# Performance work log

Measured on AMD Instinct MI355X. Metric: run time of the kernel, lower is better.

The kernel has to match this reference:

```python
import jax, jax.numpy as jnp
import numpy as np

HEADS = 8
DIM_HEAD = 64
SCALE = DIM_HEAD ** -0.5


def setup_inputs() -> dict:
    key = jax.random.key(0)
    k1, k2, k3, k4 = jax.random.split(key, 4)
    b, dim, l = 4, 512, 2048
    hidden = HEADS * DIM_HEAD  # 512
    x = jax.random.normal(k1, (b, dim, l), dtype=jnp.float32)
    w_qkv = jax.random.normal(k2, (3 * hidden, dim), dtype=jnp.float32) * (dim ** -0.5)
    w_out = jax.random.normal(k3, (dim, hidden), dtype=jnp.float32) * (hidden ** -0.5)
    b_out = jax.random.normal(k4, (dim,), dtype=jnp.float32) * 0.01
    return {"x": x, "w_qkv": w_qkv, "w_out": w_out, "b_out": b_out}


def reference(x, w_qkv, w_out, b_out):
    b, c, l = x.shape
    h, d = HEADS, DIM_HEAD
    # 1x1 Conv1d == channel matmul: [3*hidden, c] x [b, c, l] -> [b, 3*hidden, l]
    qkv = jnp.einsum('oc,bcl->bol', w_qkv, x)
    q, k, v = jnp.split(qkv, 3, axis=1)
    # 'b (h d) l -> b h d l'
    q = q.reshape(b, h, d, l) * SCALE
    k = k.reshape(b, h, d, l)
    v = v.reshape(b, h, d, l)
    sim = jnp.einsum('bhdi,bhdj->bhij', q, k)          # [b, h, l, l]
    attn = jax.nn.softmax(sim, axis=-1)
    out = jnp.einsum('bhij,bhdj->bhid', attn, v)       # [b, h, l, d]
    # 'b h l d -> b (h d) l'
    out = out.transpose(0, 1, 3, 2).reshape(b, h * d, l)
    return jnp.einsum('oc,bcl->bol', w_out, out) + b_out[None, :, None]
```

## Files before the change

kernel.cpp:

```cpp
#include <hip/hip_runtime.h>

#define L_SEQ 2048
#define KDIM  512

typedef __attribute__((ext_vector_type(8))) short short8v;
typedef __attribute__((ext_vector_type(4))) float f32x4;

static __device__ __forceinline__ short f2b(float f) {
    union { float f; unsigned u; } v; v.f = f;
    unsigned r = v.u + 0x7fffu + ((v.u >> 16) & 1u);
    return (short)(r >> 16);
}

static __device__ __forceinline__ float fast_exp2(float x) {
#if __has_builtin(__builtin_amdgcn_exp2f)
    return __builtin_amdgcn_exp2f(x);
#else
    return exp2f(x);
#endif
}

static __device__ __forceinline__ void gl2lds16(const short* g, short* l) {
    __builtin_amdgcn_global_load_lds(
        (const __attribute__((address_space(1))) unsigned*)g,
        (__attribute__((address_space(3))) unsigned*)l,
        16, 0, 0);
}

__global__ __launch_bounds__(256) void prep(
    const float* __restrict__ wq, const float* __restrict__ wo,
    const float* __restrict__ x,
    short* __restrict__ wqb, short* __restrict__ wob, short* __restrict__ xT)
{
    __shared__ __align__(16) float T[64 * 72];
    const int t = threadIdx.x;
    int bid = blockIdx.x;

    if (bid < 1024) {
        const int i = bid * 256 + t;
        const int NQ = 1536 * 512 / 4;
        float4 v;
        if (i < NQ) v = ((const float4*)wq)[i];
        else        v = ((const float4*)wo)[i - NQ];
        short4 s;
        s.x = f2b(v.x); s.y = f2b(v.y); s.z = f2b(v.z); s.w = f2b(v.w);
        if (i < NQ) ((short4*)wqb)[i] = s;
        else        ((short4*)wob)[i - NQ] = s;
        return;
    }
    bid -= 1024;
    const int l0 = (bid & 31) * 64;
    const int c0 = ((bid >> 5) & 7) * 64;
    const int b  = bid >> 8;

#pragma unroll
    for (int j = 0; j < 4; ++j) {
        const int idx = j * 256 + t;
        const int row = idx >> 4, c4 = idx & 15;
        const float4 v = *(const float4*)&x[((size_t)b * KDIM + c0 + row) * L_SEQ + l0 + c4 * 4];
        *(float4*)&T[row * 72 + c4 * 4] = v;
    }
    __syncthreads();

#pragma unroll
    for (int j = 0; j < 2; ++j) {
        const int idx = j * 256 + t;
        const int l = idx >> 3, ch = idx & 7;
        short8v s;
#pragma unroll
        for (int e = 0; e < 8; ++e)
            s[e] = f2b(T[(ch * 8 + e) * 72 + l]);
        *(short8v*)&xT[((size_t)b * L_SEQ + l0 + l) * KDIM + c0 + ch * 8] = s;
    }
}

template<int EPI>
__global__ __launch_bounds__(256) void gemm_bt(
    const short* __restrict__ Ag, const short* __restrict__ Bbase,
    const float* __restrict__ bias,
    short* __restrict__ Qws, short* __restrict__ Kws, short* __restrict__ Vws,
    float* __restrict__ Cout)
{
    constexpr int TO   = (EPI == 0) ? 128 : 64;
    constexpr int WO   = TO / 2;
    constexpr int NI   = WO / 16;
    constexpr int CA   = TO * 64 * 2 / 1024;
    constexpr int CB   = 16;
    constexpr int CPW  = (CA + CB) / 4;
    constexpr int SMEM = (EPI == 0) ? 34816 : 24576;

    const int bz = blockIdx.z;
    const int o0 = blockIdx.y * TO;
    const int l0 = blockIdx.x * 128;
    const short* Bg = Bbase + (size_t)bz * L_SEQ * KDIM;

    __shared__ __align__(16) char smem[SMEM];
    short* sA = (short*)smem;
    short* sB = (short*)(smem + TO * 64 * 2);

    const int t    = threadIdx.x;
    const int w    = t >> 6;
    const int lane = t & 63;
    const int quad = lane >> 4;
    const int l16  = lane & 15;
    const int wo   = (w & 1) * WO;
    const int wl   = (w >> 1) * 64;

    f32x4 acc[NI][4];
#pragma unroll
    for (int i = 0; i < NI; ++i)
#pragma unroll
        for (int n = 0; n < 4; ++n) acc[i][n] = (f32x4){0,0,0,0};

    const int lrow = lane >> 3;
    const int lcol = (lane & 7) * 8;

    for (int k0 = 0; k0 < KDIM; k0 += 64) {
#pragma unroll
        for (int p = 0; p < CPW; ++p) {
            const int cid = w * CPW + p;
            if (cid < CA) {
                const int row = cid * 8 + lrow;
                gl2lds16(Ag + (size_t)(o0 + row) * KDIM + k0 + lcol, sA + cid * 512);
            } else {
                const int row = (cid - CA) * 8 + lrow;
                gl2lds16(Bg + (size_t)(l0 + row) * KDIM + k0 + lcol, sB + (cid - CA) * 512);
            }
        }
        __syncthreads();

#pragma unroll
        for (int ks = 0; ks < 2; ++ks) {
            short8v af[NI], bf[4];
#pragma unroll
            for (int i = 0; i < NI; ++i)
                af[i] = *(const short8v*)&sA[(wo + i * 16 + l16) * 64 + ks * 32 + quad * 8];
#pragma unroll
            for (int n = 0; n < 4; ++n)
                bf[n] = *(const short8v*)&sB[(wl + n * 16 + l16) * 64 + ks * 32 + quad * 8];
#pragma unroll
            for (int i = 0; i < NI; ++i)
#pragma unroll
                for (int n = 0; n < 4; ++n)
                    acc[i][n] = __builtin_amdgcn_mfma_f32_16x16x32_bf16(af[i], bf[n], acc[i][n], 0, 0, 0);
        }
        __syncthreads();
    }

    if (EPI == 0) {
        const int type  = o0 >> 9;
        const int local = o0 & 511;
        const int bh0   = bz * 8 + (local >> 6);
        const float sc  = (type == 0) ? 0.18033688011112042f : 1.0f;
        short* T = (short*)smem;

        if (type == 2) {
#pragma unroll
            for (int i = 0; i < NI; ++i)
#pragma unroll
                for (int n = 0; n < 4; ++n)
#pragma unroll
                    for (int r = 0; r < 4; ++r)
                        T[(wo + i * 16 + quad * 4 + r) * 136 + wl + n * 16 + l16] =
                            f2b(acc[i][n][r]);
            __syncthreads();
#pragma unroll
            for (int p = 0; p < 8; ++p) {
                const int idx = p * 256 + t;
                const int o = idx >> 4, c = idx & 15;
                const float4 v = *(const float4*)&T[o * 136 + c * 8];
                short* dst = Vws + ((size_t)(bh0 + (o >> 6)) * 64 + (o & 63)) * L_SEQ + l0 + c * 8;
                *(float4*)dst = v;
            }
        } else {
#pragma unroll
            for (int i = 0; i < NI; ++i)
#pragma unroll
                for (int n = 0; n < 4; ++n) {
                    short4 s;
                    s.x = f2b(acc[i][n][0] * sc);
                    s.y = f2b(acc[i][n][1] * sc);
                    s.z = f2b(acc[i][n][2] * sc);
                    s.w = f2b(acc[i][n][3] * sc);
                    *(short4*)&T[(wl + n * 16 + l16) * 136 + wo + i * 16 + quad * 4] = s;
                }
            __syncthreads();
            short* base = (type == 0) ? Qws : Kws;
#pragma unroll
            for (int p = 0; p < 8; ++p) {
                const int idx = p * 256 + t;
                const int l = idx >> 4, c = idx & 15;
                const float4 v = *(const float4*)&T[l * 136 + c * 8];
                short* dst = base + ((size_t)(bh0 + (c >> 3)) * L_SEQ + l0 + l) * 64 + (c & 7) * 8;
                *(float4*)dst = v;
            }
        }
    } else {
        float* Cb = Cout + (size_t)bz * KDIM * L_SEQ;
#pragma unroll
        for (int i = 0; i < NI; ++i) {
            const int o = o0 + wo + i * 16 + quad * 4;
            float bv[4];
#pragma unroll
            for (int r = 0; r < 4; ++r) bv[r] = bias[o + r];
#pragma unroll
            for (int n = 0; n < 4; ++n) {
                const int l = l0 + wl + n * 16 + l16;
#pragma unroll
                for (int r = 0; r < 4; ++r)
                    Cb[(size_t)(o + r) * L_SEQ + l] = acc[i][n][r] + bv[r];
            }
        }
    }
}

__global__ __launch_bounds__(256) void attn_mfma(
    const short* __restrict__ Qws, const short* __restrict__ Kws,
    const short* __restrict__ Vws, short* __restrict__ ao)
{
    const int bh = blockIdx.x & 31;
    const int b  = bh >> 3;
    const int h  = bh & 7;
    const int i0 = (blockIdx.x >> 5) * 128;

    __shared__ __align__(16) char smem[36864];
    short* Kld = (short*)smem;
    short* Vld = (short*)(smem + 9216);
    short* Pld = (short*)(smem + 18432);
    float* Old = (float*)smem;

    const int t    = threadIdx.x;
    const int w    = t >> 6;
    const int lane = t & 63;
    const int quad = lane >> 4;
    const int l16  = lane & 15;

    const short* Qb = Qws + (size_t)bh * L_SEQ * 64;
    const short* Kb = Kws + (size_t)bh * L_SEQ * 64;
    const short* Vb = Vws + (size_t)bh * 64 * L_SEQ;

    short8v qa[2][2];
#pragma unroll
    for (int hh = 0; hh < 2; ++hh) {
        const short* qrow = Qb + (size_t)(i0 + w * 32 + hh * 16 + l16) * 64 + quad * 8;
        qa[hh][0] = *(const short8v*)qrow;
        qa[hh][1] = *(const short8v*)(qrow + 32);
    }

    f32x4 oacc[2][4];
#pragma unroll
    for (int hh = 0; hh < 2; ++hh)
#pragma unroll
        for (int n = 0; n < 4; ++n) oacc[hh][n] = (f32x4){0,0,0,0};
    float rsum[2] = {0.f, 0.f};
    short* Pw = Pld + w * 32 * 72;

    const int r = t >> 2, c = t & 3;

    for (int j0 = 0; j0 < L_SEQ; j0 += 64) {
        {
            const float4 k0 = *(const float4*)(Kb + (size_t)(j0 + r) * 64 + c * 16);
            const float4 k1 = *(const float4*)(Kb + (size_t)(j0 + r) * 64 + c * 16 + 8);
            const float4 v0 = *(const float4*)(Vb + (size_t)r * L_SEQ + j0 + c * 16);
            const float4 v1 = *(const float4*)(Vb + (size_t)r * L_SEQ + j0 + c * 16 + 8);
            *(float4*)&Kld[r * 72 + c * 16]     = k0;
            *(float4*)&Kld[r * 72 + c * 16 + 8] = k1;
            *(float4*)&Vld[r * 72 + c * 16]     = v0;
            *(float4*)&Vld[r * 72 + c * 16 + 8] = v1;
        }
        __syncthreads();

        f32x4 sacc[2][4];
#pragma unroll
        for (int hh = 0; hh < 2; ++hh)
#pragma unroll
            for (int n = 0; n < 4; ++n) sacc[hh][n] = (f32x4){0,0,0,0};
#pragma unroll
        for (int n = 0; n < 4; ++n) {
            short8v kf0 = *(const short8v*)&Kld[(n * 16 + l16) * 72 + quad * 8];
            short8v kf1 = *(const short8v*)&Kld[(n * 16 + l16) * 72 + 32 + quad * 8];
#pragma unroll
            for (int hh = 0; hh < 2; ++hh) {
                sacc[hh][n] = __builtin_amdgcn_mfma_f32_16x16x32_bf16(kf0, qa[hh][0], sacc[hh][n], 0, 0, 0);
                sacc[hh][n] = __builtin_amdgcn_mfma_f32_16x16x32_bf16(kf1, qa[hh][1], sacc[hh][n], 0, 0, 0);
            }
        }

#pragma unroll
        for (int hh = 0; hh < 2; ++hh)
#pragma unroll
            for (int n = 0; n < 4; ++n) {
                const float p0 = fast_exp2(sacc[hh][n][0]);
                const float p1 = fast_exp2(sacc[hh][n][1]);
                const float p2 = fast_exp2(sacc[hh][n][2]);
                const float p3 = fast_exp2(sacc[hh][n][3]);
                rsum[hh] += (p0 + p1) + (p2 + p3);
                uint2 pv;
                pv.x = __builtin_amdgcn_perm(__float_as_uint(p1), __float_as_uint(p0), 0x07060302u);
                pv.y = __builtin_amdgcn_perm(__float_as_uint(p3), __float_as_uint(p2), 0x07060302u);
                *(uint2*)&Pw[(hh * 16 + l16) * 72 + n * 16 + quad * 4] = pv;
            }

        short8v pa[2][2];
#pragma unroll
        for (int hh = 0; hh < 2; ++hh) {
            pa[hh][0] = *(const short8v*)&Pw[(hh * 16 + l16) * 72 + quad * 8];
            pa[hh][1] = *(const short8v*)&Pw[(hh * 16 + l16) * 72 + 32 + quad * 8];
        }
#pragma unroll
        for (int n = 0; n < 4; ++n) {
            short8v vf0 = *(const short8v*)&Vld[(n * 16 + l16) * 72 + quad * 8];
            short8v vf1 = *(const short8v*)&Vld[(n * 16 + l16) * 72 + 32 + quad * 8];
#pragma unroll
            for (int hh = 0; hh < 2; ++hh) {
                oacc[hh][n] = __builtin_amdgcn_mfma_f32_16x16x32_bf16(pa[hh][0], vf0, oacc[hh][n], 0, 0, 0);
                oacc[hh][n] = __builtin_amdgcn_mfma_f32_16x16x32_bf16(pa[hh][1], vf1, oacc[hh][n], 0, 0, 0);
            }
        }
        __syncthreads();
    }

    float inv[2];
#pragma unroll
    for (int hh = 0; hh < 2; ++hh) {
        rsum[hh] += __shfl_xor(rsum[hh], 16, 64);
        rsum[hh] += __shfl_xor(rsum[hh], 32, 64);
        inv[hh] = 1.0014f / rsum[hh];
    }

#pragma unroll
    for (int hh = 0; hh < 2; ++hh)
#pragma unroll
        for (int rr = 0; rr < 4; ++rr) {
            const float iv = __shfl(inv[hh], quad * 4 + rr, 64);
#pragma unroll
            for (int n = 0; n < 4; ++n)
                Old[(w * 32 + hh * 16 + quad * 4 + rr) * 68 + n * 16 + l16] =
                    oacc[hh][n][rr] * iv;
        }
    __syncthreads();
#pragma unroll
    for (int p = 0; p < 8; ++p) {
        const int idx = p * 256 + t;
        const int i = idx >> 4, c4 = idx & 15;
        const float4 v = *(const float4*)&Old[i * 68 + c4 * 4];
        short4 s;
        s.x = f2b(v.x); s.y = f2b(v.y); s.z = f2b(v.z); s.w = f2b(v.w);
        *(short4*)&ao[((size_t)b * L_SEQ + i0 + i) * KDIM + h * 64 + c4 * 4] = s;
    }
}

extern "C" void kernel_launch(void* const* d_in, const int* in_sizes, int n_in,
                              void* d_out, int out_size, void* d_ws, size_t ws_size,
                              hipStream_t stream)
{
    const float* x     = (const float*)d_in[0];
    const float* w_qkv = (const float*)d_in[1];
    const float* w_out = (const float*)d_in[2];
    const float* b_out = (const float*)d_in[3];
    float* out = (float*)d_out;

    char* ws = (char*)d_ws;
    short* xT    = (short*)ws;                      ws += (size_t)4 * L_SEQ * KDIM * 2;
    short* wq_bf = (short*)ws;                      ws += (size_t)1536 * 512 * 2;
    short* wo_bf = (short*)ws;                      ws += (size_t)512 * 512 * 2;
    short* Qws   = (short*)ws;                      ws += (size_t)32 * L_SEQ * 64 * 2;
    short* Kws   = (short*)ws;                      ws += (size_t)32 * L_SEQ * 64 * 2;
    short* Vws   = (short*)ws;                      ws += (size_t)32 * L_SEQ * 64 * 2;
    short* ao    = (short*)ws;

    dim3 blk(256);
    prep       <<<dim3(2048), blk, 0, stream>>>(w_qkv, w_out, x, wq_bf, wo_bf, xT);
    gemm_bt<0> <<<dim3(16, 12, 4), blk, 0, stream>>>(wq_bf, xT, nullptr, Qws, Kws, Vws, nullptr);
    attn_mfma  <<<dim3(512), blk, 0, stream>>>(Qws, Kws, Vws, ao);
    gemm_bt<1> <<<dim3(16, 8, 4), blk, 0, stream>>>(wo_bf, ao, b_out, nullptr, nullptr, nullptr, out);
}
```

Baseline: 168.7 us.

## Split attention over key halves with a separate combine kernel

Splits each attention block's key range into two halves, launching twice as many blocks (1024 instead of 512) so more of the GPU's compute units are occupied. Each half writes a normalized partial output in bf16 plus its row sums, and a new combine kernel merges them weighted by the row-sum ratio. This relies on the softmax using no running-max subtraction, so the two halves share a scale and can be merged directly. In exchange it adds a kernel launch, extra global traffic for the partial outputs, and an extra bf16 rounding step.

```diff
diff --git a/kernel.cpp b/kernel.cpp
--- a/kernel.cpp
+++ b/kernel.cpp
@@ -10,6 +10,11 @@
     union { float f; unsigned u; } v; v.f = f;
     unsigned r = v.u + 0x7fffu + ((v.u >> 16) & 1u);
     return (short)(r >> 16);
+}
+
+static __device__ __forceinline__ float b2f(short s) {
+    union { unsigned u; float f; } v; v.u = ((unsigned)(unsigned short)s) << 16;
+    return v.f;
 }
 
 static __device__ __forceinline__ float fast_exp2(float x) {
@@ -216,12 +221,14 @@
 
 __global__ __launch_bounds__(256) void attn_mfma(
     const short* __restrict__ Qws, const short* __restrict__ Kws,
-    const short* __restrict__ Vws, short* __restrict__ ao)
+    const short* __restrict__ Vws, short* __restrict__ Opart,
+    float* __restrict__ Rpart)
 {
     const int bh = blockIdx.x & 31;
-    const int b  = bh >> 3;
-    const int h  = bh & 7;
-    const int i0 = (blockIdx.x >> 5) * 128;
+    const int it = (blockIdx.x >> 5) & 15;
+    const int jh = blockIdx.x >> 9;
+    const int i0 = it * 128;
+    const int part = (jh << 9) | (blockIdx.x & 511);
 
     __shared__ __align__(16) char smem[36864];
     short* Kld = (short*)smem;
@@ -256,8 +263,9 @@
     short* Pw = Pld + w * 32 * 72;
 
     const int r = t >> 2, c = t & 3;
-
-    for (int j0 = 0; j0 < L_SEQ; j0 += 64) {
+    const int jbeg = jh * 1024;
+
+    for (int j0 = jbeg; j0 < jbeg + 1024; j0 += 64) {
         {
             const float4 k0 = *(const float4*)(Kb + (size_t)(j0 + r) * 64 + c * 16);
             const float4 k1 = *(const float4*)(Kb + (size_t)(j0 + r) * 64 + c * 16 + 8);
@@ -328,6 +336,12 @@
         inv[hh] = 1.0014f / rsum[hh];
     }
 
+    if (quad == 0) {
+#pragma unroll
+        for (int hh = 0; hh < 2; ++hh)
+            Rpart[(size_t)part * 128 + w * 32 + hh * 16 + l16] = rsum[hh];
+    }
+
 #pragma unroll
     for (int hh = 0; hh < 2; ++hh)
 #pragma unroll
@@ -339,6 +353,7 @@
                     oacc[hh][n][rr] * iv;
         }
     __syncthreads();
+    short* Ob = Opart + (size_t)part * 128 * 64;
 #pragma unroll
     for (int p = 0; p < 8; ++p) {
         const int idx = p * 256 + t;
@@ -346,7 +361,46 @@
         const float4 v = *(const float4*)&Old[i * 68 + c4 * 4];
         short4 s;
         s.x = f2b(v.x); s.y = f2b(v.y); s.z = f2b(v.z); s.w = f2b(v.w);
-        *(short4*)&ao[((size_t)b * L_SEQ + i0 + i) * KDIM + h * 64 + c4 * 4] = s;
+        *(short4*)&Ob[(size_t)i * 64 + c4 * 4] = s;
+    }
+}
+
+__global__ __launch_bounds__(256) void combine(
+    const short* __restrict__ Opart, const float* __restrict__ Rpart,
+    short* __restrict__ ao)
+{
+    const int id = blockIdx.x;
+    const int bh = id & 31;
+    const int it = id >> 5;
+    const int b  = bh >> 3;
+    const int h  = bh & 7;
+    const int i0 = it * 128;
+    const int t  = threadIdx.x;
+
+    __shared__ float w1s[128];
+    if (t < 128) {
+        const float r1 = Rpart[(size_t)id * 128 + t];
+        const float r2 = Rpart[(size_t)(512 + id) * 128 + t];
+        w1s[t] = r1 / (r1 + r2);
+    }
+    __syncthreads();
+
+    const short* O1 = Opart + (size_t)id * 128 * 64;
+    const short* O2 = Opart + (size_t)(512 + id) * 128 * 64;
+
+#pragma unroll
+    for (int p = 0; p < 4; ++p) {
+        const int idx = p * 256 + t;
+        const int i  = idx >> 3;
+        const int ch = (idx & 7) * 8;
+        short8v a = *(const short8v*)&O1[(size_t)i * 64 + ch];
+        short8v c = *(const short8v*)&O2[(size_t)i * 64 + ch];
+        const float w1 = w1s[i], w2 = 1.0f - w1;
+        short8v o;
+#pragma unroll
+        for (int e = 0; e < 8; ++e)
+            o[e] = f2b(w1 * b2f(a[e]) + w2 * b2f(c[e]));
+        *(short8v*)&ao[((size_t)b * L_SEQ + i0 + i) * KDIM + h * 64 + ch] = o;
     }
 }
 
@@ -367,11 +421,14 @@
     short* Qws   = (short*)ws;                      ws += (size_t)32 * L_SEQ * 64 * 2;
     short* Kws   = (short*)ws;                      ws += (size_t)32 * L_SEQ * 64 * 2;
     short* Vws   = (short*)ws;                      ws += (size_t)32 * L_SEQ * 64 * 2;
-    short* ao    = (short*)ws;
+    short* ao    = (short*)ws;                      ws += (size_t)4 * L_SEQ * KDIM * 2;
+    short* Opart = (short*)ws;                      ws += (size_t)1024 * 128 * 64 * 2;
+    float* Rpart = (float*)ws;
 
     dim3 blk(256);
     prep       <<<dim3(2048), blk, 0, stream>>>(w_qkv, w_out, x, wq_bf, wo_bf, xT);
     gemm_bt<0> <<<dim3(16, 12, 4), blk, 0, stream>>>(wq_bf, xT, nullptr, Qws, Kws, Vws, nullptr);
-    attn_mfma  <<<dim3(512), blk, 0, stream>>>(Qws, Kws, Vws, ao);
+    attn_mfma  <<<dim3(1024), blk, 0, stream>>>(Qws, Kws, Vws, Opart, Rpart);
+    combine    <<<dim3(512), blk, 0, stream>>>(Opart, Rpart, ao);
     gemm_bt<1> <<<dim3(16, 8, 4), blk, 0, stream>>>(wo_bf, ao, b_out, nullptr, nullptr, nullptr, out);
 }
```

Result: no change. 170.6 us (+1.1%).
